# Optimization experiments

Hardware: AMD Instinct MI355X
Metric: run time of the kernel (lower is better)

## Reference

```python
import jax, jax.numpy as jnp
import numpy as np

EPS = 1e-7  # K.epsilon()
ROUTINGS = 3

def squash(v):
    # v: [..., dim_capsule]
    s2 = jnp.sum(jnp.square(v), axis=-1, keepdims=True)
    scale = s2 / (1.0 + s2) / jnp.sqrt(s2 + EPS)
    return scale * v

def setup_inputs() -> dict:
    key = jax.random.key(0)
    k1, k2 = jax.random.split(key)
    B, IN_CAPS, IN_DIM = 256, 1152, 8
    NUM_CAPS, DIM_CAPS = 10, 16
    inputs = jax.random.normal(k1, (B, IN_CAPS, IN_DIM), dtype=jnp.float32)
    W = jax.random.normal(k2, (NUM_CAPS, IN_CAPS, DIM_CAPS, IN_DIM), dtype=jnp.float32) * 0.05
    return {"inputs": inputs, "W": W}

def reference(inputs, W):
    # inputs: [B, I, Q]; W: [J, I, P, Q]
    # inputs_hat[b,j,i,p] = sum_q W[j,i,p,q] * inputs[b,i,q]
    inputs_hat = jnp.einsum('jipq,biq->bjip', W, inputs)  # [B, J, I, P]
    B, J, I, P = inputs_hat.shape
    b = jnp.zeros((B, J, I), dtype=inputs_hat.dtype)
    outputs = None
    for r in range(ROUTINGS):
        c = jax.nn.softmax(b, axis=1)                      # over num_capsule J
        s = jnp.einsum('bji,bjip->bjp', c, inputs_hat)     # [B, J, P]
        outputs = squash(s)
        if r < ROUTINGS - 1:
            b = b + jnp.einsum('bjp,bjip->bji', outputs, inputs_hat)
    return outputs
```

## Files before the change

kernel.cpp:

```cpp
#include <hip/hip_runtime.h>

typedef _Float16 h2 __attribute__((ext_vector_type(2)));
typedef _Float16 h8 __attribute__((ext_vector_type(8)));
typedef float f4 __attribute__((ext_vector_type(4)));

#define BB 256
#define II 1152
#define QQ 8
#define JJ 10
#define PP 16

#define BT 16
#define IT 8
#define NBT (BB / BT)
#define NIT (II / IT)
#define XRH 72
#define WTILE (IT * PP * QQ)

#define NW (JJ * II * PP * QQ)
#define NX (BB * II * QQ)
#define NS (BB * JJ * PP)
#define LOG2E 1.4426950408889634f

template <int CTRL>
__device__ __forceinline__ float dpp_add(float v) {
    int s = __builtin_bit_cast(int, v);
    int t = __builtin_amdgcn_update_dpp(0, s, CTRL, 0xF, 0xF, true);
    return v + __builtin_bit_cast(float, t);
}
__device__ __forceinline__ float row_sum16(float v) {
    v = dpp_add<0xB1>(v);
    v = dpp_add<0x4E>(v);
    v = dpp_add<0x124>(v);
    v = dpp_add<0x128>(v);
    return v;
}
template <int CTRL>
__device__ __forceinline__ h2 dpp_add_pk(h2 v) {
    int s = __builtin_bit_cast(int, v);
    int t = __builtin_amdgcn_update_dpp(0, s, CTRL, 0xF, 0xF, true);
    return v + __builtin_bit_cast(h2, t);
}
__device__ __forceinline__ h2 row_sum16_pk(h2 v) {
    v = dpp_add_pk<0xB1>(v);
    v = dpp_add_pk<0x4E>(v);
    v = dpp_add_pk<0x124>(v);
    v = dpp_add_pk<0x128>(v);
    return v;
}

__device__ __forceinline__ float dot8(h8 w, h8 x) {
    h2 w0 = __builtin_shufflevector(w, w, 0, 1), w1 = __builtin_shufflevector(w, w, 2, 3);
    h2 w2 = __builtin_shufflevector(w, w, 4, 5), w3 = __builtin_shufflevector(w, w, 6, 7);
    h2 x0 = __builtin_shufflevector(x, x, 0, 1), x1 = __builtin_shufflevector(x, x, 2, 3);
    h2 x2 = __builtin_shufflevector(x, x, 4, 5), x3 = __builtin_shufflevector(x, x, 6, 7);
    float acc = __builtin_amdgcn_fdot2(w0, x0, 0.0f, false);
    acc = __builtin_amdgcn_fdot2(w1, x1, acc, false);
    acc = __builtin_amdgcn_fdot2(w2, x2, acc, false);
    acc = __builtin_amdgcn_fdot2(w3, x3, acc, false);
    return acc;
}

__global__ __launch_bounds__(256) void prep_kernel(
    const float* __restrict__ X, const float* __restrict__ W,
    _Float16* __restrict__ Xh, _Float16* __restrict__ Wh,
    float* __restrict__ S)
{
    const int g = blockIdx.x * 256 + threadIdx.x;
    const int stride = gridDim.x * 256;
    typedef _Float16 h4 __attribute__((ext_vector_type(4)));
    for (int k = g; k < NW / 4; k += stride) {
        const float4 f = ((const float4*)W)[k];
        h4 o = { (_Float16)f.x, (_Float16)f.y, (_Float16)f.z, (_Float16)f.w };
        ((h4*)Wh)[k] = o;
    }
    for (int k = g; k < NX / 4; k += stride) {
        const float4 f = ((const float4*)X)[k];
        h4 o = { (_Float16)f.x, (_Float16)f.y, (_Float16)f.z, (_Float16)f.w };
        ((h4*)Xh)[k] = o;
    }
    const float4 z = {0.f, 0.f, 0.f, 0.f};
    for (int k = g; k < 3 * NS / 4; k += stride) ((float4*)S)[k] = z;
}

__global__ __launch_bounds__(256) void s0_mfma_kernel(
    const _Float16* __restrict__ Xh, const _Float16* __restrict__ Wh,
    float* __restrict__ S0)
{
    const int wid  = blockIdx.x * 4 + (threadIdx.x >> 6);
    const int lane = threadIdx.x & 63;
    const int bt  = wid / 80;
    const int rem = wid % 80;
    const int j   = rem >> 3;
    const int kc  = rem & 7;
    const int b0  = bt * 16;
    const int m    = lane & 15;
    const int quad = lane >> 4;
    const int ib   = kc * 144;

    const _Float16* ax = Xh + ((size_t)(b0 + m) * II + ib + quad) * QQ;
    const _Float16* bw = Wh + (((size_t)j * II + ib + quad) * PP + m) * QQ;

    f4 acc = {0.f, 0.f, 0.f, 0.f};
    for (int t = 0; t < 36; ++t) {
        const h8 a = *(const h8*)ax;
        const h8 b = *(const h8*)bw;
        acc = __builtin_amdgcn_mfma_f32_16x16x32_f16(a, b, acc, 0, 0, 0);
        ax += 4 * QQ;
        bw += (size_t)4 * PP * QQ;
    }
#pragma unroll
    for (int r = 0; r < 4; ++r)
        atomicAdd(&S0[((size_t)(b0 + quad * 4 + r) * JJ + j) * PP + m], 0.1f * acc[r]);
}

template <int MODE>
__global__ __launch_bounds__(256) void vv_kernel(
    const float* __restrict__ S, float* __restrict__ V0raw,
    float* __restrict__ VV)
{
    const int idx = blockIdx.x * 256 + threadIdx.x;
    const float s = S[idx];
    const float n2 = row_sum16(s * s);
    const float sc = n2 * __builtin_amdgcn_rcpf(1.0f + n2)
                        * __builtin_amdgcn_rsqf(n2 + 1e-7f);
    const float v = s * sc;
    if (MODE == 0) {
        V0raw[idx] = v;
        VV[idx] = v * LOG2E;
    } else {
        VV[idx] = (v + V0raw[idx]) * LOG2E;
    }
}

__global__ __launch_bounds__(256, 4) void pass_kernel(
    const _Float16* __restrict__ Xh,
    const _Float16* __restrict__ Wh,
    const float* __restrict__ VV,
    float* __restrict__ Sout)
{
    __shared__ _Float16 ws[JJ * WTILE];
    __shared__ _Float16 xs[BT * XRH];

    const int bt = blockIdx.x & (NBT - 1);
    const int it = blockIdx.x >> 4;
    const int b0 = bt * BT;
    const int i0 = it * IT;
    const int tid = threadIdx.x;

    {
        const size_t jstride = (size_t)II * PP * QQ;
        const _Float16* wsrc = Wh + (size_t)i0 * PP * QQ;
#pragma unroll
        for (int k = 0; k < 5; ++k) {
            const int c = tid + k * 256;
            const int j = c >> 7;
            const int r = c & 127;
            *(h8*)(ws + j * WTILE + r * 8) = *(const h8*)(wsrc + j * jstride + r * 8);
        }
        if (tid < 128) {
            const int xb = tid >> 3;
            const int xr = tid & 7;
            *(h8*)(xs + xb * XRH + xr * 8) =
                *(const h8*)(Xh + ((size_t)(b0 + xb) * II + i0) * QQ + xr * 8);
        }
    }
    __syncthreads();

    const int b_l = tid >> 4;
    const int p   = tid & 15;
    const int b   = b0 + b_l;

    float vv[JJ];
#pragma unroll
    for (int j = 0; j < JJ; ++j)
        vv[j] = VV[((size_t)b * JJ + j) * PP + p];

    float sacc[JJ];
#pragma unroll
    for (int j = 0; j < JJ; ++j) sacc[j] = 0.0f;

    const _Float16* wb = ws + p * QQ;
    const _Float16* xb = xs + b_l * XRH;

#pragma unroll
    for (int i = 0; i < IT; ++i) {
        const h8 x8 = *(const h8*)(xb + i * QQ);

        float h[JJ];
#pragma unroll
        for (int j = 0; j < JJ; ++j)
            h[j] = dot8(*(const h8*)(wb + j * WTILE + i * PP * QQ), x8);

        float e[JJ];
#pragma unroll
        for (int jp = 0; jp < JJ; jp += 2) {
            const h2 pk = __builtin_bit_cast(h2,
                __builtin_amdgcn_cvt_pkrtz(vv[jp] * h[jp],
                                           vv[jp + 1] * h[jp + 1]));
            const h2 r = row_sum16_pk(pk);
            e[jp]     = __builtin_amdgcn_exp2f((float)r.x);
            e[jp + 1] = __builtin_amdgcn_exp2f((float)r.y);
        }
        float a0 = (e[0] + e[1]) + (e[2] + e[3]);
        float a1 = (e[4] + e[5]) + (e[6] + e[7]);
        const float sum = (a0 + a1) + (e[8] + e[9]);
        const float inv = __builtin_amdgcn_rcpf(sum);
#pragma unroll
        for (int j = 0; j < JJ; ++j) sacc[j] += (e[j] * inv) * h[j];
    }

#pragma unroll
    for (int j = 0; j < JJ; ++j)
        atomicAdd(&Sout[((size_t)b * JJ + j) * PP + p], sacc[j]);
}

__global__ __launch_bounds__(256) void squash_out_kernel(const float* __restrict__ S,
                                                         float* __restrict__ V)
{
    const int idx = blockIdx.x * blockDim.x + threadIdx.x;
    if (idx >= BB * JJ) return;
    const float4* sp = (const float4*)(S + idx * PP);
    float4 a = sp[0], b4 = sp[1], c4 = sp[2], d4 = sp[3];
    float s2 = a.x * a.x + a.y * a.y + a.z * a.z + a.w * a.w +
               b4.x * b4.x + b4.y * b4.y + b4.z * b4.z + b4.w * b4.w +
               c4.x * c4.x + c4.y * c4.y + c4.z * c4.z + c4.w * c4.w +
               d4.x * d4.x + d4.y * d4.y + d4.z * d4.z + d4.w * d4.w;
    const float scale = s2 / (1.0f + s2) / sqrtf(s2 + 1e-7f);
    a.x *= scale; a.y *= scale; a.z *= scale; a.w *= scale;
    b4.x *= scale; b4.y *= scale; b4.z *= scale; b4.w *= scale;
    c4.x *= scale; c4.y *= scale; c4.z *= scale; c4.w *= scale;
    d4.x *= scale; d4.y *= scale; d4.z *= scale; d4.w *= scale;
    float4* vp = (float4*)(V + idx * PP);
    vp[0] = a; vp[1] = b4; vp[2] = c4; vp[3] = d4;
}

extern "C" void kernel_launch(void* const* d_in, const int* in_sizes, int n_in,
                              void* d_out, int out_size, void* d_ws, size_t ws_size,
                              hipStream_t stream)
{
    const float* X = (const float*)d_in[0];
    const float* W = (const float*)d_in[1];
    float* out = (float*)d_out;

    _Float16* Xh = (_Float16*)d_ws;
    _Float16* Wh = Xh + NX;
    float* S0 = (float*)(Wh + NW);
    float* S1 = S0 + NS;
    float* S2 = S1 + NS;
    float* V0raw = S2 + NS;
    float* VV1   = V0raw + NS;
    float* VV2   = VV1 + NS;

    const int grid  = NBT * NIT;
    const int vgrid = NS / 256;

    prep_kernel<<<1024, 256, 0, stream>>>(X, W, Xh, Wh, S0);
    s0_mfma_kernel<<<320, 256, 0, stream>>>(Xh, Wh, S0);
    vv_kernel<0><<<vgrid, 256, 0, stream>>>(S0, V0raw, VV1);
    pass_kernel<<<grid, 256, 0, stream>>>(Xh, Wh, VV1, S1);
    vv_kernel<1><<<vgrid, 256, 0, stream>>>(S1, V0raw, VV2);
    pass_kernel<<<grid, 256, 0, stream>>>(Xh, Wh, VV2, S2);
    squash_out_kernel<<<10, 256, 0, stream>>>(S2, out);
}
```

Before: 132.0 us.

## Add transposed X layout for MFMA loads, remap pass block order, pack vv in fp16

The prep kernel now also writes an i-major transposed fp16 copy of X, so the s0 MFMA kernel's per-lane A-operand loads come from contiguous batch rows. The pass kernel remaps block indices to interleave batch tiles across groups of eight, likely for cache or XCD locality. It also pre-packs the routing vectors to fp16 pairs and multiplies in packed half precision, saving one multiply per element. The cost is an extra scattered write of X in prep, more workspace, and a slight loss of precision in the logits.

Result: no change. 132.3 us, median of 2 (+0.2%).

```diff
diff --git a/kernel.cpp b/kernel.cpp
--- a/kernel.cpp
+++ b/kernel.cpp
@@ -64,6 +64,7 @@
 __global__ __launch_bounds__(256) void prep_kernel(
     const float* __restrict__ X, const float* __restrict__ W,
     _Float16* __restrict__ Xh, _Float16* __restrict__ Wh,
+    _Float16* __restrict__ XT,
     float* __restrict__ S)
 {
     const int g = blockIdx.x * 256 + threadIdx.x;
@@ -78,13 +79,19 @@
         const float4 f = ((const float4*)X)[k];
         h4 o = { (_Float16)f.x, (_Float16)f.y, (_Float16)f.z, (_Float16)f.w };
         ((h4*)Xh)[k] = o;
+        const int e0 = k * 4;
+        const int b  = e0 / (II * QQ);
+        const int r  = e0 - b * (II * QQ);
+        const int i  = r >> 3;
+        const int q  = r & 7;
+        *(h4*)(XT + ((size_t)i * BB + b) * QQ + q) = o;
     }
     const float4 z = {0.f, 0.f, 0.f, 0.f};
     for (int k = g; k < 3 * NS / 4; k += stride) ((float4*)S)[k] = z;
 }
 
 __global__ __launch_bounds__(256) void s0_mfma_kernel(
-    const _Float16* __restrict__ Xh, const _Float16* __restrict__ Wh,
+    const _Float16* __restrict__ XT, const _Float16* __restrict__ Wh,
     float* __restrict__ S0)
 {
     const int wid  = blockIdx.x * 4 + (threadIdx.x >> 6);
@@ -98,7 +105,7 @@
     const int quad = lane >> 4;
     const int ib   = kc * 144;
 
-    const _Float16* ax = Xh + ((size_t)(b0 + m) * II + ib + quad) * QQ;
+    const _Float16* ax = XT + ((size_t)(ib + quad) * BB + b0 + m) * QQ;
     const _Float16* bw = Wh + (((size_t)j * II + ib + quad) * PP + m) * QQ;
 
     f4 acc = {0.f, 0.f, 0.f, 0.f};
@@ -106,7 +113,7 @@
         const h8 a = *(const h8*)ax;
         const h8 b = *(const h8*)bw;
         acc = __builtin_amdgcn_mfma_f32_16x16x32_f16(a, b, acc, 0, 0, 0);
-        ax += 4 * QQ;
+        ax += (size_t)4 * BB * QQ;
         bw += (size_t)4 * PP * QQ;
     }
 #pragma unroll
@@ -142,8 +149,11 @@
     __shared__ _Float16 ws[JJ * WTILE];
     __shared__ _Float16 xs[BT * XRH];
 
-    const int bt = blockIdx.x & (NBT - 1);
-    const int it = blockIdx.x >> 4;
+    const int L  = blockIdx.x;
+    const int xc = L & 7;
+    const int k8 = L >> 3;
+    const int bt = 2 * xc + (k8 & 1);
+    const int it = k8 >> 1;
     const int b0 = bt * BT;
     const int i0 = it * IT;
     const int tid = threadIdx.x;
@@ -171,10 +181,13 @@
     const int p   = tid & 15;
     const int b   = b0 + b_l;
 
-    float vv[JJ];
-#pragma unroll
-    for (int j = 0; j < JJ; ++j)
-        vv[j] = VV[((size_t)b * JJ + j) * PP + p];
+    h2 vvpk[5];
+#pragma unroll
+    for (int jp = 0; jp < JJ; jp += 2) {
+        const float v0 = VV[((size_t)b * JJ + jp) * PP + p];
+        const float v1 = VV[((size_t)b * JJ + jp + 1) * PP + p];
+        vvpk[jp >> 1] = __builtin_bit_cast(h2, __builtin_amdgcn_cvt_pkrtz(v0, v1));
+    }
 
     float sacc[JJ];
 #pragma unroll
@@ -195,10 +208,9 @@
         float e[JJ];
 #pragma unroll
         for (int jp = 0; jp < JJ; jp += 2) {
-            const h2 pk = __builtin_bit_cast(h2,
-                __builtin_amdgcn_cvt_pkrtz(vv[jp] * h[jp],
-                                           vv[jp + 1] * h[jp + 1]));
-            const h2 r = row_sum16_pk(pk);
+            const h2 hp = __builtin_bit_cast(h2,
+                __builtin_amdgcn_cvt_pkrtz(h[jp], h[jp + 1]));
+            const h2 r = row_sum16_pk(vvpk[jp >> 1] * hp);
             e[jp]     = __builtin_amdgcn_exp2f((float)r.x);
             e[jp + 1] = __builtin_amdgcn_exp2f((float)r.y);
         }
@@ -245,7 +257,8 @@
 
     _Float16* Xh = (_Float16*)d_ws;
     _Float16* Wh = Xh + NX;
-    float* S0 = (float*)(Wh + NW);
+    _Float16* XT = Wh + NW;
+    float* S0 = (float*)(XT + NX);
     float* S1 = S0 + NS;
     float* S2 = S1 + NS;
     float* V0raw = S2 + NS;
@@ -255,8 +268,8 @@
     const int grid  = NBT * NIT;
     const int vgrid = NS / 256;
 
-    prep_kernel<<<1024, 256, 0, stream>>>(X, W, Xh, Wh, S0);
-    s0_mfma_kernel<<<320, 256, 0, stream>>>(Xh, Wh, S0);
+    prep_kernel<<<1024, 256, 0, stream>>>(X, W, Xh, Wh, XT, S0);
+    s0_mfma_kernel<<<320, 256, 0, stream>>>(XT, Wh, S0);
     vv_kernel<0><<<vgrid, 256, 0, stream>>>(S0, V0raw, VV1);
     pass_kernel<<<grid, 256, 0, stream>>>(Xh, Wh, VV1, S1);
     vv_kernel<1><<<vgrid, 256, 0, stream>>>(S1, V0raw, VV2);
```
